# Kernel tuning notes

Hardware: AMD Instinct MI355X
Metric: run time of the kernel (lower is better)

Reference implementation:

```python
import jax, jax.numpy as jnp
import numpy as np

N_TOKENS = 4096
NUM_IN = 512
OUTPUT_DIMS = [512, 512, 256]
TOTAL_OUT = sum(OUTPUT_DIMS)  # 1280
N_EXPERTS = 8
TOP_K = 2
TEBD_DIM = 64
NTYPES = 128


def setup_inputs() -> dict:
    key = jax.random.key(0)
    ks = jax.random.split(key, 6)
    x = jax.random.normal(ks[0], (N_TOKENS, NUM_IN), dtype=jnp.float32)
    type_embeddings = jax.random.normal(ks[1], (NTYPES, TEBD_DIM), dtype=jnp.float32)
    atom_types = jax.random.randint(ks[2], (N_TOKENS,), 0, NTYPES)
    # learned parameters
    gate_in_dim = NUM_IN + TEBD_DIM
    W_gate = jax.random.normal(ks[3], (gate_in_dim, N_EXPERTS), dtype=jnp.float32) / np.sqrt(gate_in_dim)
    W_exp = jax.random.normal(ks[4], (N_EXPERTS, NUM_IN, TOTAL_OUT), dtype=jnp.float32) / np.sqrt(NUM_IN)
    b_exp = jax.random.normal(ks[5], (N_EXPERTS, TOTAL_OUT), dtype=jnp.float32) * 0.01
    return {"x": x, "type_embeddings": type_embeddings, "atom_types": atom_types,
            "W_gate": W_gate, "W_exp": W_exp, "b_exp": b_exp}


def reference(x, type_embeddings, atom_types, W_gate, W_exp, b_exp):
    # --- gating: atom-type-conditioned router (tebd_dim > 0) ---
    tebd = type_embeddings[atom_types]                      # [N, T]
    gate_in = jnp.concatenate([x, tebd], axis=-1)           # [N, D+T]
    logits = gate_in @ W_gate                               # [N, E]
    top_v, top_i = jax.lax.top_k(logits, TOP_K)             # [N, k]
    probs = jax.nn.softmax(top_v, axis=-1)                  # renormalized over selected experts
    # dense sparse-gate matrix [N, E] (zeros for unselected experts)
    gates = jnp.sum(jax.nn.one_hot(top_i, N_EXPERTS, dtype=x.dtype) * probs[..., None], axis=1)
    # --- expert compute (grouped GEMM expressed densely) ---
    y_all = jnp.einsum('nd,edo->neo', x, W_exp) + b_exp     # [N, E, O]
    fused = jnp.einsum('ne,neo->no', gates, y_all)          # [N, TOTAL_OUT]
    # --- split fused output per head ---
    splits = np.cumsum(OUTPUT_DIMS)[:-1].tolist()
    return tuple(jnp.split(fused, splits, axis=-1))
```

## Files before the change

kernel.cpp:

```cpp
#include <hip/hip_runtime.h>
#include <hip/hip_bf16.h>
#include <cstdint>
#include <cmath>

#define NT 4096
#define DIN 512
#define DOUT 1280
#define NE 8
#define TDIM 64
#define MAXTILES 80
#define NB 10
#define GATE_BLOCKS (NT / 4)
#define CONVW_BLOCKS (20 * (DIN / 64) * NE)
#define S1ROWS 5120

typedef __attribute__((ext_vector_type(8))) short bhalf8;
typedef __attribute__((ext_vector_type(4))) float f32x4;

__device__ __forceinline__ unsigned short f2bf(float f) {
    __hip_bfloat16 h = __float2bfloat16(f);
    return *reinterpret_cast<unsigned short*>(&h);
}

__device__ __forceinline__ void gatomic_fadd(float* p, float v) {
    asm volatile("global_atomic_add_f32 %0, %1, off" : : "v"(p), "v"(v) : "memory");
}

__device__ __forceinline__ void glds16(const unsigned short* g, unsigned short* l) {
    __builtin_amdgcn_global_load_lds(
        (const __attribute__((address_space(1))) void*)g,
        (__attribute__((address_space(3))) void*)l, 16, 0, 0);
}

__global__ __launch_bounds__(256) void prep_kernel(
    const float* __restrict__ x, const float* __restrict__ temb,
    const int* __restrict__ atype, const float* __restrict__ Wg,
    const float* __restrict__ W,
    unsigned short* __restrict__ xb, unsigned short* __restrict__ WT,
    int* __restrict__ e0a, int* __restrict__ e1a,
    float* __restrict__ g0a, float* __restrict__ g1a,
    float* __restrict__ out, int zero_out)
{
    __shared__ unsigned short t[64 * 72];
    const int tid = threadIdx.x;

    if ((int)blockIdx.x < GATE_BLOCKS) {
        const int n = blockIdx.x * 4 + (tid >> 6);
        const int l = tid & 63;

        if (zero_out) {
            const f32x4 z = (f32x4){0.f, 0.f, 0.f, 0.f};
            f32x4* o0 = reinterpret_cast<f32x4*>(out + (size_t)n * 512);
            f32x4* o1 = reinterpret_cast<f32x4*>(out + (size_t)NT * 512 + (size_t)n * 512);
            f32x4* o2 = reinterpret_cast<f32x4*>(out + (size_t)NT * 1024 + (size_t)n * 256);
            o0[l] = z; o0[l + 64] = z;
            o1[l] = z; o1[l + 64] = z;
            o2[l] = z;
        }

        float acc[NE];
#pragma unroll
        for (int e = 0; e < NE; ++e) acc[e] = 0.f;

        const float* xr = x + (size_t)n * DIN;
#pragma unroll
        for (int i = 0; i < DIN / 64; ++i) {
            const int k = i * 64 + l;
            const float xv = xr[k];
            xb[(size_t)n * DIN + k] = f2bf(xv);
            const float* wr = Wg + (size_t)k * NE;
#pragma unroll
            for (int e = 0; e < NE; ++e) acc[e] = fmaf(xv, wr[e], acc[e]);
        }
        {
            const int tt = atype[n];
            const float tv = temb[(size_t)tt * TDIM + l];
            const float* wr = Wg + (size_t)(DIN + l) * NE;
#pragma unroll
            for (int e = 0; e < NE; ++e) acc[e] = fmaf(tv, wr[e], acc[e]);
        }
#pragma unroll
        for (int off = 32; off > 0; off >>= 1) {
#pragma unroll
            for (int e = 0; e < NE; ++e) acc[e] += __shfl_xor(acc[e], off, 64);
        }
        if (l == 0) {
            int e0 = 0; float v0 = acc[0];
#pragma unroll
            for (int e = 1; e < NE; ++e) if (acc[e] > v0) { v0 = acc[e]; e0 = e; }
            int e1 = -1; float v1 = -INFINITY;
#pragma unroll
            for (int e = 0; e < NE; ++e) {
                if (e == e0) continue;
                if (acc[e] > v1) { v1 = acc[e]; e1 = e; }
            }
            const float p1 = expf(v1 - v0);
            const float s  = 1.f + p1;
            e0a[n] = e0; e1a[n] = e1; g0a[n] = 1.f / s; g1a[n] = p1 / s;
        }
    } else {
        const int b  = blockIdx.x - GATE_BLOCKS;
        const int n0 = (b % 20) * 64;
        const int k0 = ((b / 20) % (DIN / 64)) * 64;
        const int e  = b / (20 * (DIN / 64));
        const int nl = tid & 63;
        const int kb = tid >> 6;
#pragma unroll
        for (int r = 0; r < 16; ++r) {
            const int kl = r * 4 + kb;
            t[nl * 72 + kl] = f2bf(W[((size_t)e * DIN + k0 + kl) * DOUT + n0 + nl]);
        }
        __syncthreads();
        const int nw = tid >> 2;
        const int kc = tid & 3;
        uint4* dst = reinterpret_cast<uint4*>(
            WT + ((size_t)e * DOUT + n0 + nw) * DIN + k0 + kc * 16);
        const uint4* src = reinterpret_cast<const uint4*>(&t[nw * 72 + kc * 16]);
        dst[0] = src[0];
        dst[1] = src[1];
    }
}

#define SORT_T 1024
__global__ __launch_bounds__(1024) void sort_kernel(
    const int* __restrict__ e0a, const int* __restrict__ e1a,
    const float* __restrict__ g0a, const float* __restrict__ g1a,
    int* __restrict__ perm, float* __restrict__ pgate,
    int* __restrict__ tile_group, int* __restrict__ ipos1,
    int* __restrict__ meta2)
{
    __shared__ int hist[16 * SORT_T];
    __shared__ int gtot[16], gbase[16];
    const int t = threadIdx.x;
    for (int i = t; i < MAXTILES * 128; i += SORT_T) { perm[i] = 0; pgate[i] = 0.f; }
#pragma unroll
    for (int g = 0; g < 16; ++g) hist[g * SORT_T + t] = 0;
    __syncthreads();

    const int nbase = t * 4;
    int keys[8];
#pragma unroll
    for (int i = 0; i < 4; ++i) {
        const int n = nbase + i;
        keys[2 * i]     = e0a[n];
        keys[2 * i + 1] = 8 + e1a[n];
    }
#pragma unroll
    for (int i = 0; i < 8; ++i) hist[keys[i] * SORT_T + t] += 1;
    __syncthreads();

    const int w = t >> 6, l = t & 63;
    {
        int running = 0;
        for (int c = 0; c < SORT_T / 64; ++c) {
            int v = hist[w * SORT_T + c * 64 + l];
            int inc = v;
#pragma unroll
            for (int d = 1; d < 64; d <<= 1) {
                int u = __shfl_up(inc, d, 64);
                if (l >= d) inc += u;
            }
            hist[w * SORT_T + c * 64 + l] = running + inc - v;
            running += __shfl(inc, 63, 64);
        }
        if (l == 0) gtot[w] = running;
    }
    __syncthreads();
    if (t == 0) {
        int s = 0;
#pragma unroll
        for (int g = 0; g < 16; ++g) {
            gbase[g] = s;
            const int ntg = (gtot[g] + 127) >> 7;
            for (int k = 0; k < ntg; ++k) tile_group[s / 128 + k] = g;
            s += ntg * 128;
        }
        meta2[0] = s / 128;
        meta2[1] = gbase[8];
    }
    __syncthreads();

#pragma unroll
    for (int i = 0; i < 4; ++i) {
        const int n = nbase + i;
        {
            const int k = keys[2 * i];
            const int pos = gbase[k] + hist[k * SORT_T + t]++;
            perm[pos] = n; pgate[pos] = g0a[n];
        }
        {
            const int k = keys[2 * i + 1];
            const int pos = gbase[k] + hist[k * SORT_T + t]++;
            perm[pos] = n; pgate[pos] = g1a[n];
            ipos1[n] = pos - gbase[8];
        }
    }
}

__device__ __forceinline__ int swz(int row, int chunk) {
    return row * 64 + ((chunk ^ (row & 7)) << 3);
}

template<int STAGEPATH>
__global__ __launch_bounds__(256, 4) void gemm_kernel(
    const unsigned short* __restrict__ Xb,
    const unsigned short* __restrict__ WT,
    const float* __restrict__ bexp,
    const int* __restrict__ perm, const float* __restrict__ pgate,
    const int* __restrict__ tile_group, const int* __restrict__ meta2,
    float* __restrict__ stage, float* __restrict__ out)
{
    constexpr int NWG = MAXTILES * NB, CPX = NWG / 8;
    const int gid = blockIdx.x;
    const int wid = (gid & 7) * CPX + (gid >> 3);
    const int tile = wid / NB, nb = wid % NB;
    if (tile >= meta2[0]) return;
    const int g  = tile_group[tile];
    const int e  = g & 7;
    const bool s1 = (g >= 8);
    const int n0 = nb * 128;

    __shared__ unsigned short As[128 * 64];
    __shared__ unsigned short Bs[128 * 64];
    __shared__ int   toks[128];
    __shared__ float gts[128];

    const int tid = threadIdx.x;
    if (tid < 128) {
        toks[tid] = perm[tile * 128 + tid];
        gts[tid]  = pgate[tile * 128 + tid];
    }
    __syncthreads();

    const int l = tid & 63;
    const int w = tid >> 6;
    const int lrow = l >> 3;
    const int schk = (l & 7) ^ lrow;

    const unsigned short* asrc[4];
    unsigned short* aldsb[4];
#pragma unroll
    for (int i = 0; i < 4; ++i) {
        asrc[i]  = Xb + (size_t)toks[i * 32 + w * 8 + lrow] * DIN + schk * 8;
        aldsb[i] = &As[(i * 32 + w * 8) * 64];
    }
    const unsigned short* bsrc[4];
    unsigned short* bldsb[4];
#pragma unroll
    for (int j = 0; j < 4; ++j) {
        bsrc[j]  = WT + ((size_t)e * DOUT + n0 + j * 32 + w * 8 + lrow) * DIN + schk * 8;
        bldsb[j] = &Bs[(j * 32 + w * 8) * 64];
    }

    f32x4 acc[4][4];
#pragma unroll
    for (int a = 0; a < 4; ++a)
#pragma unroll
        for (int b = 0; b < 4; ++b) acc[a][b] = (f32x4){0.f, 0.f, 0.f, 0.f};

    const int wm = w >> 1, wn = w & 1;
    const int fr = l & 15;
    const int fh = l >> 4;

    for (int k0 = 0; k0 < DIN; k0 += 64) {
        __syncthreads();
#pragma unroll
        for (int i = 0; i < 4; ++i) glds16(asrc[i] + k0, aldsb[i]);
#pragma unroll
        for (int j = 0; j < 4; ++j) glds16(bsrc[j] + k0, bldsb[j]);
        __syncthreads();
#pragma unroll
        for (int ks = 0; ks < 2; ++ks) {
            bhalf8 af[4], bff[4];
#pragma unroll
            for (int fm = 0; fm < 4; ++fm)
                af[fm] = *reinterpret_cast<const bhalf8*>(
                    &As[swz(wm * 64 + fm * 16 + fr, ks * 4 + fh)]);
#pragma unroll
            for (int fn = 0; fn < 4; ++fn)
                bff[fn] = *reinterpret_cast<const bhalf8*>(
                    &Bs[swz(wn * 64 + fn * 16 + fr, ks * 4 + fh)]);
#pragma unroll
            for (int fm = 0; fm < 4; ++fm)
#pragma unroll
                for (int fn = 0; fn < 4; ++fn)
                    acc[fm][fn] = __builtin_amdgcn_mfma_f32_16x16x32_bf16(
                        af[fm], bff[fn], acc[fm][fn], 0, 0, 0);
        }
    }

    size_t base; int width, cstart;
    if (n0 < 512)       { base = 0;                 width = 512; cstart = n0; }
    else if (n0 < 1024) { base = (size_t)NT * 512;  width = 512; cstart = n0 - 512; }
    else                { base = (size_t)NT * 1024; width = 256; cstart = n0 - 1024; }
    const int lc = l & 15, lr = l >> 4;
    float bval[4];
#pragma unroll
    for (int fn = 0; fn < 4; ++fn)
        bval[fn] = bexp[(size_t)e * DOUT + n0 + wn * 64 + fn * 16 + lc];

    if (STAGEPATH && s1) {
        const int srow0 = tile * 128 - meta2[1];
#pragma unroll
        for (int fm = 0; fm < 4; ++fm) {
#pragma unroll
            for (int j = 0; j < 4; ++j) {
                const int row = wm * 64 + fm * 16 + lr * 4 + j;
                const float gg = gts[row];
                float* sp = stage + (size_t)(srow0 + row) * DOUT + n0 + wn * 64 + lc;
#pragma unroll
                for (int fn = 0; fn < 4; ++fn)
                    sp[fn * 16] = gg * (acc[fm][fn][j] + bval[fn]);
            }
        }
    } else {
        const int coloff = cstart + wn * 64 + lc;
#pragma unroll
        for (int fm = 0; fm < 4; ++fm) {
#pragma unroll
            for (int j = 0; j < 4; ++j) {
                const int row = wm * 64 + fm * 16 + lr * 4 + j;
                const float gg = gts[row];
                if (gg != 0.f) {
                    float* op = out + base + (size_t)toks[row] * width + coloff;
#pragma unroll
                    for (int fn = 0; fn < 4; ++fn) {
                        const float v = gg * (acc[fm][fn][j] + bval[fn]);
                        if (STAGEPATH) op[fn * 16] = v;
                        else           gatomic_fadd(op + fn * 16, v);
                    }
                }
            }
        }
    }
}

__global__ __launch_bounds__(256) void combine_kernel(
    const float* __restrict__ stage, const int* __restrict__ ipos1,
    float* __restrict__ out)
{
    const int n = blockIdx.x;
    const int t = threadIdx.x;
    const size_t r = (size_t)ipos1[n] * DOUT;
#pragma unroll
    for (int k = 0; k < 5; ++k) {
        const int c = t + k * 256;
        const float v = stage[r + c];
        float* p;
        if (k < 2)      p = out + (size_t)n * 512 + c;
        else if (k < 4) p = out + (size_t)NT * 512 + (size_t)n * 512 + (c - 512);
        else            p = out + (size_t)NT * 1024 + (size_t)n * 256 + (c - 1024);
        *p += v;
    }
}

extern "C" void kernel_launch(void* const* d_in, const int* in_sizes, int n_in,
                              void* d_out, int out_size, void* d_ws, size_t ws_size,
                              hipStream_t stream) {
    const float* x     = (const float*)d_in[0];
    const float* temb  = (const float*)d_in[1];
    const int*   atype = (const int*)d_in[2];
    const float* Wg    = (const float*)d_in[3];
    const float* Wexp  = (const float*)d_in[4];
    const float* bexp  = (const float*)d_in[5];
    float* out = (float*)d_out;
    char*  ws  = (char*)d_ws;

    unsigned short* xb = (unsigned short*)(ws);
    unsigned short* wt = (unsigned short*)(ws + (size_t)4194304);
    float* stage = (float*)(ws + (size_t)14680064);
    const size_t META = 14680064 + (size_t)S1ROWS * DOUT * 4;
    char* meta = ws + META;
    int*   e0a = (int*)(meta);
    int*   e1a = (int*)(meta + 16384);
    float* g0a = (float*)(meta + 32768);
    float* g1a = (float*)(meta + 49152);
    int*   perm       = (int*)(meta + 65536);
    float* pgate      = (float*)(meta + 106496);
    int*   tile_group = (int*)(meta + 147456);
    int*   ipos1      = (int*)(meta + 147968);
    int*   meta2      = (int*)(meta + 164352);

    const bool use_stage = (ws_size >= META + 165000);

    prep_kernel<<<dim3(GATE_BLOCKS + CONVW_BLOCKS), dim3(256), 0, stream>>>(
        x, temb, atype, Wg, Wexp, xb, wt, e0a, e1a, g0a, g1a, out,
        use_stage ? 0 : 1);
    sort_kernel<<<dim3(1), dim3(SORT_T), 0, stream>>>(
        e0a, e1a, g0a, g1a, perm, pgate, tile_group, ipos1, meta2);
    if (use_stage) {
        gemm_kernel<1><<<dim3(MAXTILES * NB), dim3(256), 0, stream>>>(
            xb, wt, bexp, perm, pgate, tile_group, meta2, stage, out);
        combine_kernel<<<dim3(NT), dim3(256), 0, stream>>>(stage, ipos1, out);
    } else {
        gemm_kernel<0><<<dim3(MAXTILES * NB), dim3(256), 0, stream>>>(
            xb, wt, bexp, perm, pgate, tile_group, meta2, stage, out);
    }
}
```

Measured before the change: 62.82 us.

## Replace staging buffer and combine kernel with two-pass GEMM read-modify-write

After: 77.09 us. +22.7%, slower.

```diff
diff --git a/kernel.cpp b/kernel.cpp
--- a/kernel.cpp
+++ b/kernel.cpp
@@ -12,7 +12,6 @@
 #define NB 10
 #define GATE_BLOCKS (NT / 4)
 #define CONVW_BLOCKS (20 * (DIN / 64) * NE)
-#define S1ROWS 5120
 
 typedef __attribute__((ext_vector_type(8))) short bhalf8;
 typedef __attribute__((ext_vector_type(4))) float f32x4;
@@ -20,10 +19,6 @@
 __device__ __forceinline__ unsigned short f2bf(float f) {
     __hip_bfloat16 h = __float2bfloat16(f);
     return *reinterpret_cast<unsigned short*>(&h);
-}
-
-__device__ __forceinline__ void gatomic_fadd(float* p, float v) {
-    asm volatile("global_atomic_add_f32 %0, %1, off" : : "v"(p), "v"(v) : "memory");
 }
 
 __device__ __forceinline__ void glds16(const unsigned short* g, unsigned short* l) {
@@ -38,8 +33,7 @@
     const float* __restrict__ W,
     unsigned short* __restrict__ xb, unsigned short* __restrict__ WT,
     int* __restrict__ e0a, int* __restrict__ e1a,
-    float* __restrict__ g0a, float* __restrict__ g1a,
-    float* __restrict__ out, int zero_out)
+    float* __restrict__ g0a, float* __restrict__ g1a)
 {
     __shared__ unsigned short t[64 * 72];
     const int tid = threadIdx.x;
@@ -47,16 +41,6 @@
     if ((int)blockIdx.x < GATE_BLOCKS) {
         const int n = blockIdx.x * 4 + (tid >> 6);
         const int l = tid & 63;
-
-        if (zero_out) {
-            const f32x4 z = (f32x4){0.f, 0.f, 0.f, 0.f};
-            f32x4* o0 = reinterpret_cast<f32x4*>(out + (size_t)n * 512);
-            f32x4* o1 = reinterpret_cast<f32x4*>(out + (size_t)NT * 512 + (size_t)n * 512);
-            f32x4* o2 = reinterpret_cast<f32x4*>(out + (size_t)NT * 1024 + (size_t)n * 256);
-            o0[l] = z; o0[l + 64] = z;
-            o1[l] = z; o1[l + 64] = z;
-            o2[l] = z;
-        }
 
         float acc[NE];
 #pragma unroll
@@ -126,8 +110,7 @@
     const int* __restrict__ e0a, const int* __restrict__ e1a,
     const float* __restrict__ g0a, const float* __restrict__ g1a,
     int* __restrict__ perm, float* __restrict__ pgate,
-    int* __restrict__ tile_group, int* __restrict__ ipos1,
-    int* __restrict__ meta2)
+    int* __restrict__ tile_group, int* __restrict__ meta2)
 {
     __shared__ int hist[16 * SORT_T];
     __shared__ int gtot[16], gbase[16];
@@ -176,7 +159,6 @@
             s += ntg * 128;
         }
         meta2[0] = s / 128;
-        meta2[1] = gbase[8];
     }
     __syncthreads();
 
@@ -192,7 +174,6 @@
             const int k = keys[2 * i + 1];
             const int pos = gbase[k] + hist[k * SORT_T + t]++;
             perm[pos] = n; pgate[pos] = g1a[n];
-            ipos1[n] = pos - gbase[8];
         }
     }
 }
@@ -201,23 +182,23 @@
     return row * 64 + ((chunk ^ (row & 7)) << 3);
 }
 
-template<int STAGEPATH>
+template<int PASS>
 __global__ __launch_bounds__(256, 4) void gemm_kernel(
     const unsigned short* __restrict__ Xb,
     const unsigned short* __restrict__ WT,
     const float* __restrict__ bexp,
     const int* __restrict__ perm, const float* __restrict__ pgate,
     const int* __restrict__ tile_group, const int* __restrict__ meta2,
-    float* __restrict__ stage, float* __restrict__ out)
+    float* __restrict__ out)
 {
     constexpr int NWG = MAXTILES * NB, CPX = NWG / 8;
     const int gid = blockIdx.x;
     const int wid = (gid & 7) * CPX + (gid >> 3);
     const int tile = wid / NB, nb = wid % NB;
     if (tile >= meta2[0]) return;
-    const int g  = tile_group[tile];
+    const int g = tile_group[tile];
+    if ((g >> 3) != PASS) return;
     const int e  = g & 7;
-    const bool s1 = (g >= 8);
     const int n0 = nb * 128;
 
     __shared__ unsigned short As[128 * 64];
@@ -294,63 +275,27 @@
     else if (n0 < 1024) { base = (size_t)NT * 512;  width = 512; cstart = n0 - 512; }
     else                { base = (size_t)NT * 1024; width = 256; cstart = n0 - 1024; }
     const int lc = l & 15, lr = l >> 4;
+    const int coloff = cstart + wn * 64 + lc;
     float bval[4];
 #pragma unroll
     for (int fn = 0; fn < 4; ++fn)
         bval[fn] = bexp[(size_t)e * DOUT + n0 + wn * 64 + fn * 16 + lc];
-
-    if (STAGEPATH && s1) {
-        const int srow0 = tile * 128 - meta2[1];
-#pragma unroll
-        for (int fm = 0; fm < 4; ++fm) {
-#pragma unroll
-            for (int j = 0; j < 4; ++j) {
-                const int row = wm * 64 + fm * 16 + lr * 4 + j;
-                const float gg = gts[row];
-                float* sp = stage + (size_t)(srow0 + row) * DOUT + n0 + wn * 64 + lc;
-#pragma unroll
-                for (int fn = 0; fn < 4; ++fn)
-                    sp[fn * 16] = gg * (acc[fm][fn][j] + bval[fn]);
-            }
-        }
-    } else {
-        const int coloff = cstart + wn * 64 + lc;
-#pragma unroll
-        for (int fm = 0; fm < 4; ++fm) {
-#pragma unroll
-            for (int j = 0; j < 4; ++j) {
-                const int row = wm * 64 + fm * 16 + lr * 4 + j;
-                const float gg = gts[row];
-                if (gg != 0.f) {
-                    float* op = out + base + (size_t)toks[row] * width + coloff;
-#pragma unroll
-                    for (int fn = 0; fn < 4; ++fn) {
-                        const float v = gg * (acc[fm][fn][j] + bval[fn]);
-                        if (STAGEPATH) op[fn * 16] = v;
-                        else           gatomic_fadd(op + fn * 16, v);
-                    }
+#pragma unroll
+    for (int fm = 0; fm < 4; ++fm) {
+#pragma unroll
+        for (int j = 0; j < 4; ++j) {
+            const int row = wm * 64 + fm * 16 + lr * 4 + j;
+            const float gg = gts[row];
+            if (gg != 0.f) {
+                float* op = out + base + (size_t)toks[row] * width + coloff;
+#pragma unroll
+                for (int fn = 0; fn < 4; ++fn) {
+                    const float v = gg * (acc[fm][fn][j] + bval[fn]);
+                    if (PASS == 0) op[fn * 16] = v;
+                    else           op[fn * 16] += v;
                 }
             }
         }
-    }
-}
-
-__global__ __launch_bounds__(256) void combine_kernel(
-    const float* __restrict__ stage, const int* __restrict__ ipos1,
-    float* __restrict__ out)
-{
-    const int n = blockIdx.x;
-    const int t = threadIdx.x;
-    const size_t r = (size_t)ipos1[n] * DOUT;
-#pragma unroll
-    for (int k = 0; k < 5; ++k) {
-        const int c = t + k * 256;
-        const float v = stage[r + c];
-        float* p;
-        if (k < 2)      p = out + (size_t)n * 512 + c;
-        else if (k < 4) p = out + (size_t)NT * 512 + (size_t)n * 512 + (c - 512);
-        else            p = out + (size_t)NT * 1024 + (size_t)n * 256 + (c - 1024);
-        *p += v;
     }
 }
 
@@ -368,9 +313,7 @@
 
     unsigned short* xb = (unsigned short*)(ws);
     unsigned short* wt = (unsigned short*)(ws + (size_t)4194304);
-    float* stage = (float*)(ws + (size_t)14680064);
-    const size_t META = 14680064 + (size_t)S1ROWS * DOUT * 4;
-    char* meta = ws + META;
+    char* meta = ws + (size_t)14680064;
     int*   e0a = (int*)(meta);
     int*   e1a = (int*)(meta + 16384);
     float* g0a = (float*)(meta + 32768);
@@ -378,22 +321,14 @@
     int*   perm       = (int*)(meta + 65536);
     float* pgate      = (float*)(meta + 106496);
     int*   tile_group = (int*)(meta + 147456);
-    int*   ipos1      = (int*)(meta + 147968);
-    int*   meta2      = (int*)(meta + 164352);
-
-    const bool use_stage = (ws_size >= META + 165000);
+    int*   meta2      = (int*)(meta + 147968);
 
     prep_kernel<<<dim3(GATE_BLOCKS + CONVW_BLOCKS), dim3(256), 0, stream>>>(
-        x, temb, atype, Wg, Wexp, xb, wt, e0a, e1a, g0a, g1a, out,
-        use_stage ? 0 : 1);
+        x, temb, atype, Wg, Wexp, xb, wt, e0a, e1a, g0a, g1a);
     sort_kernel<<<dim3(1), dim3(SORT_T), 0, stream>>>(
-        e0a, e1a, g0a, g1a, perm, pgate, tile_group, ipos1, meta2);
-    if (use_stage) {
-        gemm_kernel<1><<<dim3(MAXTILES * NB), dim3(256), 0, stream>>>(
-            xb, wt, bexp, perm, pgate, tile_group, meta2, stage, out);
-        combine_kernel<<<dim3(NT), dim3(256), 0, stream>>>(stage, ipos1, out);
-    } else {
-        gemm_kernel<0><<<dim3(MAXTILES * NB), dim3(256), 0, stream>>>(
-            xb, wt, bexp, perm, pgate, tile_group, meta2, stage, out);
-    }
-}
+        e0a, e1a, g0a, g1a, perm, pgate, tile_group, meta2);
+    gemm_kernel<0><<<dim3(MAXTILES * NB), dim3(256), 0, stream>>>(
+        xb, wt, bexp, perm, pgate, tile_group, meta2, out);
+    gemm_kernel<1><<<dim3(MAXTILES * NB), dim3(256), 0, stream>>>(
+        xb, wt, bexp, perm, pgate, tile_group, meta2, out);
+}
```
